# Kernel tuning notes

Hardware: AMD Instinct MI355X
Metric: run time of the kernel (lower is better)

Reference implementation:

```python
import jax, jax.numpy as jnp
import numpy as np


def setup_inputs() -> dict:
    key = jax.random.key(0)
    ks = jax.random.split(key, 3)
    B, H, W, C = 32, 56, 56, 512
    N = H * W
    x = jax.random.normal(ks[0], (B, N, C), dtype=jnp.float32)
    # learned params (qkv_bias=False)
    w_qkv = jax.random.normal(ks[1], (C, 3 * C), dtype=jnp.float32) * (C ** -0.5)
    w_proj = jax.random.normal(ks[2], (C, C), dtype=jnp.float32) * (C ** -0.5)
    b_proj = jnp.zeros((C,), dtype=jnp.float32)
    return {"x": x, "w_qkv": w_qkv, "w_proj": w_proj, "b_proj": b_proj,
            "H": H, "W": W}


def reference(x, w_qkv, w_proj, b_proj, H, W):
    num_heads, ws = 8, 7
    B, N, C = x.shape
    hd = C // num_heads
    scale = hd ** -0.5
    hg, wg = H // ws, W // ws
    G = hg * wg  # total groups
    S = ws * ws  # tokens per window
    # window partition: [B,N,C] -> [B,G,S,C]
    xw = x.reshape(B, hg, ws, wg, ws, C).transpose(0, 1, 3, 2, 4, 5)
    xw = xw.reshape(B, G, S, C)
    # qkv projection -> [3,B,G,heads,S,hd]
    qkv = (xw @ w_qkv).reshape(B, G, S, 3, num_heads, hd)
    qkv = qkv.transpose(3, 0, 1, 4, 2, 5)
    q, k, v = qkv[0], qkv[1], qkv[2]
    attn = jnp.einsum('bghqd,bghkd->bghqk', q, k) * scale
    attn = jax.nn.softmax(attn, axis=-1)
    out = jnp.einsum('bghqk,bghkd->bghqd', attn, v)
    # merge heads: [B,G,h,S,d] -> [B,G,S,C]
    out = out.transpose(0, 1, 3, 2, 4).reshape(B, G, S, C)
    # window merge: [B,G,S,C] -> [B,N,C]
    out = out.reshape(B, hg, wg, ws, ws, C).transpose(0, 1, 3, 2, 4, 5)
    out = out.reshape(B, N, C)
    return out @ w_proj + b_proj
```

## Files before the change

### kernel.cpp

```cpp
#include <hip/hip_runtime.h>

typedef unsigned short ushort;
typedef unsigned int uint;
typedef __bf16 bf16x8 __attribute__((ext_vector_type(8)));
typedef unsigned short u16x8 __attribute__((ext_vector_type(8)));
typedef float f32x4 __attribute__((ext_vector_type(4)));

__device__ __forceinline__ ushort f2bf(float f) {
  uint u = __builtin_bit_cast(uint, f);
  u += 0x7fffu + ((u >> 16) & 1u);
  return (ushort)(u >> 16);
}

__device__ __forceinline__ f32x4 mfma_bf16(u16x8 a, u16x8 b, f32x4 c) {
  return __builtin_amdgcn_mfma_f32_16x16x32_bf16(
      __builtin_bit_cast(bf16x8, a), __builtin_bit_cast(bf16x8, b), c, 0, 0, 0);
}

__device__ __forceinline__ uint win2orig(uint wr) {
  uint b = wr / 3136u, rem = wr % 3136u;
  uint g = rem / 49u, s = rem % 49u;
  return b * 3136u + ((g >> 3) * 7u + s / 7u) * 56u + (g & 7u) * 7u + s % 7u;
}

__global__ __launch_bounds__(256) void cvt_x_win(const float* __restrict__ X,
                                                 ushort* __restrict__ Xb, int total8) {
  int stride = gridDim.x * 256;
  for (int i = blockIdx.x * 256 + threadIdx.x; i < total8; i += stride) {
    uint wr = (uint)i >> 6, c8 = (uint)i & 63u;
    const float* xp = X + (size_t)win2orig(wr) * 512 + c8 * 8;
    f32x4 a = *(const f32x4*)xp;
    f32x4 b = *(const f32x4*)(xp + 4);
    u16x8 o;
#pragma unroll
    for (int j = 0; j < 4; ++j) { o[j] = f2bf(a[j]); o[j + 4] = f2bf(b[j]); }
    ((u16x8*)Xb)[i] = o;
  }
}

__global__ __launch_bounds__(256) void transpose_cvt(const float* __restrict__ W,
                                                     ushort* __restrict__ WT,
                                                     int K, int N) {
  __shared__ float t[32][33];
  const int tn0 = blockIdx.x * 32, tk0 = blockIdx.y * 32;
  const int tx = threadIdx.x & 31, ty = threadIdx.x >> 5;
#pragma unroll
  for (int i = 0; i < 4; ++i) {
    int k = tk0 + ty + i * 8;
    t[ty + i * 8][tx] = W[(size_t)k * N + tn0 + tx];
  }
  __syncthreads();
#pragma unroll
  for (int i = 0; i < 4; ++i) {
    int n = tn0 + ty + i * 8;
    WT[(size_t)n * K + tk0 + tx] = f2bf(t[tx][ty + i * 8]);
  }
}


#define GLL(g, l)                                                              \
  __builtin_amdgcn_global_load_lds(                                            \
      (const __attribute__((address_space(1))) uint*)(g),                      \
      (__attribute__((address_space(3))) uint*)(l), 16, 0, 0)
#define BAR() __builtin_amdgcn_s_barrier()
#define SCB() __builtin_amdgcn_sched_barrier(0)
#define WAITV(n) asm volatile("s_waitcnt vmcnt(" #n ")" ::: "memory")

template <int OUT>
__global__ __launch_bounds__(512, 2) void gemm8p(const ushort* __restrict__ A,
                                                 const ushort* __restrict__ BT,
                                                 void* __restrict__ Cout,
                                                 const float* __restrict__ bias,
                                                 const int ldc, const int NT,
                                                 const int CPX) {
  __shared__ __align__(16) ushort as_[2][16384];
  __shared__ __align__(16) ushort bs_[2][16384];
  const int bid = blockIdx.x;
  const int wg = (bid & 7) * CPX + (bid >> 3);
  const int mt = wg / NT, nt = wg - mt * NT;
  const int m0 = mt << 8, n0 = nt << 8;
  const int tid = threadIdx.x, lane = tid & 63, wid = tid >> 6;
  const int wm = wid >> 2, wn = wid & 3;
  const int c16 = lane & 15, q4 = lane >> 4;
  const int sw = c16 & 7;
  const int lrow = lane >> 3, lcg = (lane & 7) ^ lrow;
  const ushort* Ag = A + (size_t)(m0 + wid * 16 + lrow) * 512 + lcg * 8;
  const ushort* Bg = BT + (size_t)(n0 + wid * 16 + lrow) * 512 + lcg * 8;
  const int aro = (wm * 64 + c16) * 64;
  const int bro = (wn * 32 + c16) * 64;
  const int ag0 = (q4 ^ sw) * 8;
  const int ag1 = ((4 + q4) ^ sw) * 8;

  f32x4 acc[8][4];
#pragma unroll
  for (int m = 0; m < 8; ++m)
#pragma unroll
    for (int n = 0; n < 4; ++n) acc[m][n] = f32x4{0.f, 0.f, 0.f, 0.f};
  u16x8 af[4][2], bf0[2][2], bf1[2][2];

#define STAGE_A(half, ktg)                                                     \
  do {                                                                         \
    const ushort* g_ = Ag + (size_t)(half) * (128 * 512) + (ktg) * 64;         \
    ushort* l_ = &as_[(ktg) & 1][(half) * 8192 + wid * 1024 + lane * 8];       \
    GLL(g_, l_);                                                               \
    GLL(g_ + 8 * 512, l_ + 512);                                               \
  } while (0)
#define STAGE_B(half, ktg)                                                     \
  do {                                                                         \
    const ushort* g_ = Bg + (size_t)(half) * (128 * 512) + (ktg) * 64;         \
    ushort* l_ = &bs_[(ktg) & 1][(half) * 8192 + wid * 1024 + lane * 8];       \
    GLL(g_, l_);                                                               \
    GLL(g_ + 8 * 512, l_ + 512);                                               \
  } while (0)
#define LDA(kt, mh)                                                            \
  do {                                                                         \
    const ushort* p_ = &as_[kt][(mh)*8192 + aro];                              \
    _Pragma("unroll") for (int f_ = 0; f_ < 4; ++f_) {                         \
      af[f_][0] = *(const u16x8*)(p_ + f_ * 1024 + ag0);                       \
      af[f_][1] = *(const u16x8*)(p_ + f_ * 1024 + ag1);                       \
    }                                                                          \
  } while (0)
#define LDB(kt, nh, BF)                                                        \
  do {                                                                         \
    const ushort* p_ = &bs_[kt][(nh)*8192 + bro];                              \
    _Pragma("unroll") for (int g_ = 0; g_ < 2; ++g_) {                         \
      BF[g_][0] = *(const u16x8*)(p_ + g_ * 1024 + ag0);                       \
      BF[g_][1] = *(const u16x8*)(p_ + g_ * 1024 + ag1);                       \
    }                                                                          \
  } while (0)
#define MM(mh, nh, BF)                                                         \
  do {                                                                         \
    __builtin_amdgcn_s_setprio(1);                                             \
    _Pragma("unroll") for (int f_ = 0; f_ < 4; ++f_)                           \
        _Pragma("unroll") for (int g_ = 0; g_ < 2; ++g_) {                     \
      f32x4& a_ = acc[(mh)*4 + f_][(nh)*2 + g_];                               \
      a_ = mfma_bf16(af[f_][0], BF[g_][0], a_);                                \
      a_ = mfma_bf16(af[f_][1], BF[g_][1], a_);                                \
    }                                                                          \
    __builtin_amdgcn_s_setprio(0);                                             \
  } while (0)

  STAGE_A(0, 0); STAGE_B(0, 0); STAGE_B(1, 0); STAGE_A(1, 0);
  STAGE_A(0, 1); STAGE_B(0, 1); STAGE_B(1, 1);
  WAITV(10); BAR(); SCB();

  for (int i = 0; i < 3; ++i) {
    const int o1 = 2 * i + 1, e2 = 2 * i + 2, o3 = 2 * i + 3;
    LDA(0, 0); LDB(0, 0, bf0); STAGE_A(1, o1);
    BAR(); MM(0, 0, bf0); WAITV(10); BAR(); SCB();
    LDB(0, 1, bf1); STAGE_A(0, e2);
    BAR(); MM(0, 1, bf1); WAITV(10); BAR(); SCB();
    LDA(0, 1); STAGE_B(0, e2);
    BAR(); MM(1, 1, bf1); BAR(); SCB();
    STAGE_B(1, e2);
    BAR(); MM(1, 0, bf0); WAITV(10); BAR(); SCB();
    LDA(1, 0); LDB(1, 0, bf0); STAGE_A(1, e2);
    BAR(); MM(0, 0, bf0); WAITV(10); BAR(); SCB();
    LDB(1, 1, bf1); STAGE_A(0, o3);
    BAR(); MM(0, 1, bf1); WAITV(10); BAR(); SCB();
    LDA(1, 1); STAGE_B(0, o3);
    BAR(); MM(1, 1, bf1); BAR(); SCB();
    STAGE_B(1, o3);
    BAR(); MM(1, 0, bf0); WAITV(10); BAR(); SCB();
  }
  LDA(0, 0); LDB(0, 0, bf0); STAGE_A(1, 7);
  BAR(); MM(0, 0, bf0); WAITV(10); BAR(); SCB();
  LDB(0, 1, bf1);
  BAR(); MM(0, 1, bf1); WAITV(8); BAR(); SCB();
  LDA(0, 1);
  BAR(); MM(1, 1, bf1); BAR(); SCB();
  BAR(); MM(1, 0, bf0); WAITV(4); BAR(); SCB();
  LDA(1, 0); LDB(1, 0, bf0);
  BAR(); MM(0, 0, bf0); WAITV(2); BAR(); SCB();
  LDB(1, 1, bf1);
  BAR(); MM(0, 1, bf1); WAITV(0); BAR(); SCB();
  LDA(1, 1);
  BAR(); MM(1, 1, bf1); BAR(); SCB();
  BAR(); MM(1, 0, bf0);

  const int crow = m0 + wm * 64 + q4 * 4;
  const int ccol = n0 + wn * 32 + c16;
  if constexpr (OUT == 0) {
    ushort* C = (ushort*)Cout;
#pragma unroll
    for (int mf = 0; mf < 8; ++mf) {
      const int ro = (mf >> 2) * 128 + (mf & 3) * 16;
#pragma unroll
      for (int r = 0; r < 4; ++r) {
        ushort* cp = C + (size_t)(crow + ro + r) * ldc + ccol;
        cp[0]   = f2bf(acc[mf][0][r]);
        cp[16]  = f2bf(acc[mf][1][r]);
        cp[128] = f2bf(acc[mf][2][r]);
        cp[144] = f2bf(acc[mf][3][r]);
      }
    }
  } else {
    float* C = (float*)Cout;
    const float b0 = bias[ccol], b1 = bias[ccol + 16];
    const float b2 = bias[ccol + 128], b3 = bias[ccol + 144];
#pragma unroll
    for (int mf = 0; mf < 8; ++mf) {
      const int ro = (mf >> 2) * 128 + (mf & 3) * 16;
#pragma unroll
      for (int r = 0; r < 4; ++r) {
        float* cp = C + (size_t)win2orig((uint)(crow + ro + r)) * 512 + ccol;
        cp[0]   = acc[mf][0][r] + b0;
        cp[16]  = acc[mf][1][r] + b1;
        cp[128] = acc[mf][2][r] + b2;
        cp[144] = acc[mf][3][r] + b3;
      }
    }
  }
#undef STAGE_A
#undef STAGE_B
#undef LDA
#undef LDB
#undef MM
}

__global__ __launch_bounds__(128) void attn_win(const ushort* __restrict__ qkv,
                                                ushort* __restrict__ O) {
  __shared__ __align__(16) ushort p_lds[2][4096];
  __shared__ __align__(16) ushort v_lds[2][4096];
  const int tid = threadIdx.x, lane = tid & 63, w = tid >> 6;
  const int wg = blockIdx.x * 2 + w;
  const int head = wg & 7, g = (wg >> 3) & 63, b = wg >> 9;
  const int c16 = lane & 15, q4 = lane >> 4;
  const size_t wrow = (size_t)b * 3136 + g * 49;
  const u16x8 Z = {0, 0, 0, 0, 0, 0, 0, 0};

  const int qc = head * 64 + q4 * 8;
  u16x8 qf[2][4], kf[2][4];
#pragma unroll
  for (int i = 0; i < 4; ++i) {
    int s = i * 16 + c16;
    bool val = (s < 49);
    const ushort* p = qkv + (wrow + (val ? s : 0)) * 1536 + qc;
#pragma unroll
    for (int kk = 0; kk < 2; ++kk) {
      qf[kk][i] = val ? *reinterpret_cast<const u16x8*>(p + kk * 32) : Z;
      kf[kk][i] = val ? *reinterpret_cast<const u16x8*>(p + 512 + kk * 32) : Z;
    }
  }

  {
    const ushort* vp = qkv + (wrow + (lane < 49 ? lane : 0)) * 1536 + 1024 + head * 64;
    u16x8 vr[8];
#pragma unroll
    for (int j = 0; j < 8; ++j)
      vr[j] = (lane < 49) ? *reinterpret_cast<const u16x8*>(vp + j * 8) : Z;
#pragma unroll
    for (int d = 0; d < 64; ++d)
      v_lds[w][(d * 64 + lane) ^ ((d & 7) << 3)] = vr[d >> 3][d & 7];
  }

  f32x4 acc[4][4];
#pragma unroll
  for (int m = 0; m < 4; ++m)
#pragma unroll
    for (int n = 0; n < 4; ++n) acc[m][n] = f32x4{0.f, 0.f, 0.f, 0.f};
  __builtin_amdgcn_s_setprio(1);
#pragma unroll
  for (int kk = 0; kk < 2; ++kk)
#pragma unroll
    for (int m = 0; m < 4; ++m)
#pragma unroll
      for (int n = 0; n < 4; ++n)
        acc[m][n] = mfma_bf16(qf[kk][m], kf[kk][n], acc[m][n]);
  __builtin_amdgcn_s_setprio(0);

#pragma unroll
  for (int m = 0; m < 4; ++m)
#pragma unroll
    for (int r = 0; r < 4; ++r) {
      float s0 = acc[m][0][r] * 0.125f;
      float s1 = acc[m][1][r] * 0.125f;
      float s2 = acc[m][2][r] * 0.125f;
      float s3 = (c16 == 0) ? acc[m][3][r] * 0.125f : -1e30f;
      float mx = fmaxf(fmaxf(s0, s1), fmaxf(s2, s3));
#pragma unroll
      for (int off = 1; off < 16; off <<= 1) mx = fmaxf(mx, __shfl_xor(mx, off));
      s0 = __expf(s0 - mx);
      s1 = __expf(s1 - mx);
      s2 = __expf(s2 - mx);
      s3 = (c16 == 0) ? __expf(s3 - mx) : 0.f;
      float sum = s0 + s1 + s2 + s3;
#pragma unroll
      for (int off = 1; off < 16; off <<= 1) sum += __shfl_xor(sum, off);
      float inv = 1.f / sum;
      int row = m * 16 + q4 * 4 + r;
      int rb = row * 64, swz = (row & 7) << 3;
      p_lds[w][(rb + c16) ^ swz]      = f2bf(s0 * inv);
      p_lds[w][(rb + 16 + c16) ^ swz] = f2bf(s1 * inv);
      p_lds[w][(rb + 32 + c16) ^ swz] = f2bf(s2 * inv);
      p_lds[w][(rb + 48 + c16) ^ swz] = f2bf(s3 * inv);
    }

  f32x4 o[4][4];
#pragma unroll
  for (int m = 0; m < 4; ++m)
#pragma unroll
    for (int n = 0; n < 4; ++n) o[m][n] = f32x4{0.f, 0.f, 0.f, 0.f};
#pragma unroll
  for (int kk = 0; kk < 2; ++kk) {
    u16x8 pa[4], vb[4];
#pragma unroll
    for (int m = 0; m < 4; ++m) {
      int row = m * 16 + c16;
      pa[m] = *reinterpret_cast<const u16x8*>(
          &p_lds[w][(row * 64 + kk * 32 + q4 * 8) ^ ((row & 7) << 3)]);
    }
#pragma unroll
    for (int n = 0; n < 4; ++n) {
      int d = n * 16 + c16;
      vb[n] = *reinterpret_cast<const u16x8*>(
          &v_lds[w][(d * 64 + kk * 32 + q4 * 8) ^ ((d & 7) << 3)]);
    }
    __builtin_amdgcn_s_setprio(1);
#pragma unroll
    for (int m = 0; m < 4; ++m)
#pragma unroll
      for (int n = 0; n < 4; ++n) o[m][n] = mfma_bf16(pa[m], vb[n], o[m][n]);
    __builtin_amdgcn_s_setprio(0);
  }

#pragma unroll
  for (int m = 0; m < 4; ++m)
#pragma unroll
    for (int r = 0; r < 4; ++r) {
      int s = m * 16 + q4 * 4 + r;
      if (s < 49) {
        ushort* op = O + (wrow + s) * 512 + head * 64 + c16;
        op[0]  = f2bf(o[m][0][r]);
        op[16] = f2bf(o[m][1][r]);
        op[32] = f2bf(o[m][2][r]);
        op[48] = f2bf(o[m][3][r]);
      }
    }
}

extern "C" void kernel_launch(void* const* d_in, const int* in_sizes, int n_in,
                              void* d_out, int out_size, void* d_ws, size_t ws_size,
                              hipStream_t stream) {
  const float* x      = (const float*)d_in[0];
  const float* w_qkv  = (const float*)d_in[1];
  const float* w_proj = (const float*)d_in[2];
  const float* b_proj = (const float*)d_in[3];
  char* ws = (char*)d_ws;
  ushort* wqkvT  = (ushort*)ws;
  ushort* wprojT = (ushort*)(ws + 1572864);
  ushort* xb     = (ushort*)(ws + 2097152);
  ushort* qkv    = (ushort*)(ws + 104857600);
  float* out = (float*)d_out;

  transpose_cvt<<<dim3(48, 16), 256, 0, stream>>>(w_qkv, wqkvT, 512, 1536);
  transpose_cvt<<<dim3(16, 16), 256, 0, stream>>>(w_proj, wprojT, 512, 512);
  cvt_x_win<<<2048, 256, 0, stream>>>(x, xb, 100352 * 512 / 8);
  gemm8p<0><<<2352, 512, 0, stream>>>(xb, wqkvT, (void*)qkv, nullptr, 1536, 6, 294);
  attn_win<<<8192, 128, 0, stream>>>(qkv, xb);
  gemm8p<1><<<784, 512, 0, stream>>>(xb, wprojT, (void*)out, b_proj, 512, 2, 98);
}
```

Baseline: 493.2 us.

## Replace 256x256 LDS GEMM with 128x128 tile loading B directly to registers

Swaps the 8-wave 256x256-tile GEMM, which staged both A and B through double-buffered LDS with a hand-tuned ping-pong schedule, for a 4-wave 128x128-tile kernel. Only A is staged through LDS, double-buffered with global_load_lds. Each wave reads its B fragments straight from global memory into registers. The smaller LDS footprint and smaller tile allow more blocks per CU and a simpler pipeline. In exchange, arithmetic intensity per tile drops, B is re-read from global/L2 by every block, and the kernel waits on all loads (vmcnt 0) each k-step, which reduces overlap.

```diff
diff --git a/kernel.cpp b/kernel.cpp
--- a/kernel.cpp
+++ b/kernel.cpp
@@ -64,158 +64,122 @@
       (__attribute__((address_space(3))) uint*)(l), 16, 0, 0)
 #define BAR() __builtin_amdgcn_s_barrier()
 #define SCB() __builtin_amdgcn_sched_barrier(0)
-#define WAITV(n) asm volatile("s_waitcnt vmcnt(" #n ")" ::: "memory")
+#define WAITV0() asm volatile("s_waitcnt vmcnt(0)" ::: "memory")
 
 template <int OUT>
-__global__ __launch_bounds__(512, 2) void gemm8p(const ushort* __restrict__ A,
-                                                 const ushort* __restrict__ BT,
-                                                 void* __restrict__ Cout,
-                                                 const float* __restrict__ bias,
-                                                 const int ldc, const int NT,
-                                                 const int CPX) {
-  __shared__ __align__(16) ushort as_[2][16384];
-  __shared__ __align__(16) ushort bs_[2][16384];
+__global__ __launch_bounds__(256, 4) void gemm_bl2(const ushort* __restrict__ A,
+                                                   const ushort* __restrict__ BT,
+                                                   void* __restrict__ Cout,
+                                                   const float* __restrict__ bias,
+                                                   const int ldc, const int NT,
+                                                   const int CPX) {
+  __shared__ __align__(16) ushort as_[2][8192];
   const int bid = blockIdx.x;
   const int wg = (bid & 7) * CPX + (bid >> 3);
   const int mt = wg / NT, nt = wg - mt * NT;
-  const int m0 = mt << 8, n0 = nt << 8;
+  const int m0 = mt << 7, n0 = nt << 7;
   const int tid = threadIdx.x, lane = tid & 63, wid = tid >> 6;
-  const int wm = wid >> 2, wn = wid & 3;
+  const int wm = wid >> 1, wn = wid & 1;
   const int c16 = lane & 15, q4 = lane >> 4;
   const int sw = c16 & 7;
-  const int lrow = lane >> 3, lcg = (lane & 7) ^ lrow;
-  const ushort* Ag = A + (size_t)(m0 + wid * 16 + lrow) * 512 + lcg * 8;
-  const ushort* Bg = BT + (size_t)(n0 + wid * 16 + lrow) * 512 + lcg * 8;
-  const int aro = (wm * 64 + c16) * 64;
-  const int bro = (wn * 32 + c16) * 64;
+
+  const ushort* Ag = A + (size_t)(m0 + (tid >> 3)) * 512 +
+                     ((tid & 7) ^ ((tid >> 3) & 7)) * 8;
+  const ushort* Bg0 = BT + (size_t)(n0 + wn * 64 + c16) * 512 + q4 * 8;
+  const ushort* Bg1 = Bg0 + (size_t)16 * 512;
+  const ushort* Bg2 = Bg0 + (size_t)32 * 512;
+  const ushort* Bg3 = Bg0 + (size_t)48 * 512;
+
+  const int aro = wm * 64 + c16;
   const int ag0 = (q4 ^ sw) * 8;
   const int ag1 = ((4 + q4) ^ sw) * 8;
 
-  f32x4 acc[8][4];
-#pragma unroll
-  for (int m = 0; m < 8; ++m)
+  f32x4 acc[4][4];
+#pragma unroll
+  for (int m = 0; m < 4; ++m)
 #pragma unroll
     for (int n = 0; n < 4; ++n) acc[m][n] = f32x4{0.f, 0.f, 0.f, 0.f};
-  u16x8 af[4][2], bf0[2][2], bf1[2][2];
-
-#define STAGE_A(half, ktg)                                                     \
+
+#define STAGE(buf, ktg)                                                        \
   do {                                                                         \
-    const ushort* g_ = Ag + (size_t)(half) * (128 * 512) + (ktg) * 64;         \
-    ushort* l_ = &as_[(ktg) & 1][(half) * 8192 + wid * 1024 + lane * 8];       \
-    GLL(g_, l_);                                                               \
-    GLL(g_ + 8 * 512, l_ + 512);                                               \
+    _Pragma("unroll") for (int j_ = 0; j_ < 4; ++j_)                           \
+        GLL(Ag + (size_t)j_ * (32 * 512) + (ktg)*64,                           \
+            &as_[buf][j_ * 2048 + tid * 8]);                                   \
   } while (0)
-#define STAGE_B(half, ktg)                                                     \
-  do {                                                                         \
-    const ushort* g_ = Bg + (size_t)(half) * (128 * 512) + (ktg) * 64;         \
-    ushort* l_ = &bs_[(ktg) & 1][(half) * 8192 + wid * 1024 + lane * 8];       \
-    GLL(g_, l_);                                                               \
-    GLL(g_ + 8 * 512, l_ + 512);                                               \
-  } while (0)
-#define LDA(kt, mh)                                                            \
-  do {                                                                         \
-    const ushort* p_ = &as_[kt][(mh)*8192 + aro];                              \
-    _Pragma("unroll") for (int f_ = 0; f_ < 4; ++f_) {                         \
-      af[f_][0] = *(const u16x8*)(p_ + f_ * 1024 + ag0);                       \
-      af[f_][1] = *(const u16x8*)(p_ + f_ * 1024 + ag1);                       \
-    }                                                                          \
-  } while (0)
-#define LDB(kt, nh, BF)                                                        \
-  do {                                                                         \
-    const ushort* p_ = &bs_[kt][(nh)*8192 + bro];                              \
-    _Pragma("unroll") for (int g_ = 0; g_ < 2; ++g_) {                         \
-      BF[g_][0] = *(const u16x8*)(p_ + g_ * 1024 + ag0);                       \
-      BF[g_][1] = *(const u16x8*)(p_ + g_ * 1024 + ag1);                       \
-    }                                                                          \
-  } while (0)
-#define MM(mh, nh, BF)                                                         \
-  do {                                                                         \
-    __builtin_amdgcn_s_setprio(1);                                             \
-    _Pragma("unroll") for (int f_ = 0; f_ < 4; ++f_)                           \
-        _Pragma("unroll") for (int g_ = 0; g_ < 2; ++g_) {                     \
-      f32x4& a_ = acc[(mh)*4 + f_][(nh)*2 + g_];                               \
-      a_ = mfma_bf16(af[f_][0], BF[g_][0], a_);                                \
-      a_ = mfma_bf16(af[f_][1], BF[g_][1], a_);                                \
-    }                                                                          \
-    __builtin_amdgcn_s_setprio(0);                                             \
-  } while (0)
-
-  STAGE_A(0, 0); STAGE_B(0, 0); STAGE_B(1, 0); STAGE_A(1, 0);
-  STAGE_A(0, 1); STAGE_B(0, 1); STAGE_B(1, 1);
-  WAITV(10); BAR(); SCB();
-
-  for (int i = 0; i < 3; ++i) {
-    const int o1 = 2 * i + 1, e2 = 2 * i + 2, o3 = 2 * i + 3;
-    LDA(0, 0); LDB(0, 0, bf0); STAGE_A(1, o1);
-    BAR(); MM(0, 0, bf0); WAITV(10); BAR(); SCB();
-    LDB(0, 1, bf1); STAGE_A(0, e2);
-    BAR(); MM(0, 1, bf1); WAITV(10); BAR(); SCB();
-    LDA(0, 1); STAGE_B(0, e2);
-    BAR(); MM(1, 1, bf1); BAR(); SCB();
-    STAGE_B(1, e2);
-    BAR(); MM(1, 0, bf0); WAITV(10); BAR(); SCB();
-    LDA(1, 0); LDB(1, 0, bf0); STAGE_A(1, e2);
-    BAR(); MM(0, 0, bf0); WAITV(10); BAR(); SCB();
-    LDB(1, 1, bf1); STAGE_A(0, o3);
-    BAR(); MM(0, 1, bf1); WAITV(10); BAR(); SCB();
-    LDA(1, 1); STAGE_B(0, o3);
-    BAR(); MM(1, 1, bf1); BAR(); SCB();
-    STAGE_B(1, o3);
-    BAR(); MM(1, 0, bf0); WAITV(10); BAR(); SCB();
-  }
-  LDA(0, 0); LDB(0, 0, bf0); STAGE_A(1, 7);
-  BAR(); MM(0, 0, bf0); WAITV(10); BAR(); SCB();
-  LDB(0, 1, bf1);
-  BAR(); MM(0, 1, bf1); WAITV(8); BAR(); SCB();
-  LDA(0, 1);
-  BAR(); MM(1, 1, bf1); BAR(); SCB();
-  BAR(); MM(1, 0, bf0); WAITV(4); BAR(); SCB();
-  LDA(1, 0); LDB(1, 0, bf0);
-  BAR(); MM(0, 0, bf0); WAITV(2); BAR(); SCB();
-  LDB(1, 1, bf1);
-  BAR(); MM(0, 1, bf1); WAITV(0); BAR(); SCB();
-  LDA(1, 1);
-  BAR(); MM(1, 1, bf1); BAR(); SCB();
-  BAR(); MM(1, 0, bf0);
+
+  STAGE(0, 0);
+  WAITV0();
+
+#pragma unroll
+  for (int kt = 0; kt < 8; ++kt) {
+    BAR();
+    u16x8 bf[2][4];
+#pragma unroll
+    for (int kk = 0; kk < 2; ++kk) {
+      bf[kk][0] = *(const u16x8*)(Bg0 + kt * 64 + kk * 32);
+      bf[kk][1] = *(const u16x8*)(Bg1 + kt * 64 + kk * 32);
+      bf[kk][2] = *(const u16x8*)(Bg2 + kt * 64 + kk * 32);
+      bf[kk][3] = *(const u16x8*)(Bg3 + kt * 64 + kk * 32);
+    }
+    SCB();
+    if (kt < 7) STAGE((kt + 1) & 1, kt + 1);
+    SCB();
+    const ushort* ab = &as_[kt & 1][0];
+    u16x8 af0[4];
+#pragma unroll
+    for (int f = 0; f < 4; ++f)
+      af0[f] = *(const u16x8*)(ab + (aro + f * 16) * 64 + ag0);
+    __builtin_amdgcn_s_setprio(1);
+#pragma unroll
+    for (int m = 0; m < 4; ++m)
+#pragma unroll
+      for (int n = 0; n < 4; ++n)
+        acc[m][n] = mfma_bf16(af0[m], bf[0][n], acc[m][n]);
+    __builtin_amdgcn_s_setprio(0);
+    u16x8 af1[4];
+#pragma unroll
+    for (int f = 0; f < 4; ++f)
+      af1[f] = *(const u16x8*)(ab + (aro + f * 16) * 64 + ag1);
+    __builtin_amdgcn_s_setprio(1);
+#pragma unroll
+    for (int m = 0; m < 4; ++m)
+#pragma unroll
+      for (int n = 0; n < 4; ++n)
+        acc[m][n] = mfma_bf16(af1[m], bf[1][n], acc[m][n]);
+    __builtin_amdgcn_s_setprio(0);
+    WAITV0();
+  }
+#undef STAGE
 
   const int crow = m0 + wm * 64 + q4 * 4;
-  const int ccol = n0 + wn * 32 + c16;
+  const int ccol = n0 + wn * 64 + c16;
   if constexpr (OUT == 0) {
     ushort* C = (ushort*)Cout;
 #pragma unroll
-    for (int mf = 0; mf < 8; ++mf) {
-      const int ro = (mf >> 2) * 128 + (mf & 3) * 16;
+    for (int m = 0; m < 4; ++m)
 #pragma unroll
       for (int r = 0; r < 4; ++r) {
-        ushort* cp = C + (size_t)(crow + ro + r) * ldc + ccol;
-        cp[0]   = f2bf(acc[mf][0][r]);
-        cp[16]  = f2bf(acc[mf][1][r]);
-        cp[128] = f2bf(acc[mf][2][r]);
-        cp[144] = f2bf(acc[mf][3][r]);
+        ushort* cp = C + (size_t)(crow + m * 16 + r) * ldc + ccol;
+        cp[0]  = f2bf(acc[m][0][r]);
+        cp[16] = f2bf(acc[m][1][r]);
+        cp[32] = f2bf(acc[m][2][r]);
+        cp[48] = f2bf(acc[m][3][r]);
       }
-    }
   } else {
     float* C = (float*)Cout;
     const float b0 = bias[ccol], b1 = bias[ccol + 16];
-    const float b2 = bias[ccol + 128], b3 = bias[ccol + 144];
-#pragma unroll
-    for (int mf = 0; mf < 8; ++mf) {
-      const int ro = (mf >> 2) * 128 + (mf & 3) * 16;
+    const float b2 = bias[ccol + 32], b3 = bias[ccol + 48];
+#pragma unroll
+    for (int m = 0; m < 4; ++m)
 #pragma unroll
       for (int r = 0; r < 4; ++r) {
-        float* cp = C + (size_t)win2orig((uint)(crow + ro + r)) * 512 + ccol;
-        cp[0]   = acc[mf][0][r] + b0;
-        cp[16]  = acc[mf][1][r] + b1;
-        cp[128] = acc[mf][2][r] + b2;
-        cp[144] = acc[mf][3][r] + b3;
+        float* cp = C + (size_t)win2orig((uint)(crow + m * 16 + r)) * 512 + ccol;
+        cp[0]  = acc[m][0][r] + b0;
+        cp[16] = acc[m][1][r] + b1;
+        cp[32] = acc[m][2][r] + b2;
+        cp[48] = acc[m][3][r] + b3;
       }
-    }
-  }
-#undef STAGE_A
-#undef STAGE_B
-#undef LDA
-#undef LDB
-#undef MM
+  }
 }
 
 __global__ __launch_bounds__(128) void attn_win(const ushort* __restrict__ qkv,
@@ -356,7 +320,7 @@
   transpose_cvt<<<dim3(48, 16), 256, 0, stream>>>(w_qkv, wqkvT, 512, 1536);
   transpose_cvt<<<dim3(16, 16), 256, 0, stream>>>(w_proj, wprojT, 512, 512);
   cvt_x_win<<<2048, 256, 0, stream>>>(x, xb, 100352 * 512 / 8);
-  gemm8p<0><<<2352, 512, 0, stream>>>(xb, wqkvT, (void*)qkv, nullptr, 1536, 6, 294);
+  gemm_bl2<0><<<9408, 256, 0, stream>>>(xb, wqkvT, (void*)qkv, nullptr, 1536, 12, 1176);
   attn_win<<<8192, 128, 0, stream>>>(qkv, xb);
-  gemm8p<1><<<784, 512, 0, stream>>>(xb, wprojT, (void*)out, b_proj, 512, 2, 98);
-}
+  gemm_bl2<1><<<3136, 256, 0, stream>>>(xb, wprojT, (void*)out, b_proj, 512, 4, 392);
+}
```

Result: slower. 648.2 us (+31.4%).
